# Performance work log

Hardware: AMD Instinct MI355X
Metric: run time of the kernel (lower is better)

## Reference

```python
import jax, jax.numpy as jnp
import numpy as np

N = 50000       # nodes
E = 800000      # edges (before self-loops)
F = 128         # input features
H = 4           # heads
C = 64          # hidden per head
NC = 40         # classes
NEG_SLOPE = 0.2  # PyG GATConv default leaky relu slope


def _glorot(key, shape):
    fan = sum(shape[-2:]) if len(shape) >= 2 else shape[-1] * 2
    return jax.random.normal(key, shape, jnp.float32) * jnp.sqrt(2.0 / fan)


def gat_conv(x, W, a_src, a_dst, bias, src, dst, concat):
    """PyG-style GATConv (eval mode, self-loops already in src/dst).
    x:[N,Fin] W:[Fin,H*C] a_src,a_dst:[H,C] bias:[H*C] or [C]."""
    n = x.shape[0]
    h_, c_ = a_src.shape
    h = (x @ W).reshape(n, h_, c_)                      # [N,H,C]
    al_s = jnp.einsum('nhc,hc->nh', h, a_src)           # [N,H]
    al_d = jnp.einsum('nhc,hc->nh', h, a_dst)
    logits = jax.nn.leaky_relu(al_s[src] + al_d[dst], NEG_SLOPE)  # [E,H]
    # segment softmax over incoming edges of each dst node
    mx = jax.ops.segment_max(logits, dst, num_segments=n)
    mx = jnp.where(jnp.isfinite(mx), mx, 0.0)
    ex = jnp.exp(logits - mx[dst])
    den = jax.ops.segment_sum(ex, dst, num_segments=n)
    alpha = ex / (den[dst] + 1e-16)                     # [E,H]
    msg = h[src] * alpha[:, :, None]                    # [E,H,C]
    out = jax.ops.segment_sum(msg, dst, num_segments=n) # [N,H,C]
    if concat:
        return out.reshape(n, h_ * c_) + bias
    return out.mean(axis=1) + bias


def setup_inputs() -> dict:
    key = jax.random.key(0)
    ks = jax.random.split(key, 16)
    x = jax.random.normal(ks[0], (N, F), jnp.float32)
    edge_index = jax.random.randint(ks[1], (2, E), 0, N, jnp.int64)
    HC = H * C
    return {
        'x': x, 'edge_index': edge_index,
        'W1': _glorot(ks[2], (F, HC)),   'a1_src': _glorot(ks[3], (H, C)),
        'a1_dst': _glorot(ks[4], (H, C)), 'b1': jnp.zeros((HC,), jnp.float32),
        'W2': _glorot(ks[5], (HC, HC)),  'a2_src': _glorot(ks[6], (H, C)),
        'a2_dst': _glorot(ks[7], (H, C)), 'b2': jnp.zeros((HC,), jnp.float32),
        'W3': _glorot(ks[8], (HC, H * NC)), 'a3_src': _glorot(ks[9], (H, NC)),
        'a3_dst': _glorot(ks[10], (H, NC)), 'b3': jnp.zeros((NC,), jnp.float32),
    }


def reference(x, edge_index, W1, a1_src, a1_dst, b1, W2, a2_src, a2_dst, b2,
              W3, a3_src, a3_dst, b3):
    n = x.shape[0]
    loop = jnp.arange(n, dtype=edge_index.dtype)
    src = jnp.concatenate([edge_index[0], loop])
    dst = jnp.concatenate([edge_index[1], loop])
    x1 = jax.nn.elu(gat_conv(x, W1, a1_src, a1_dst, b1, src, dst, True))
    x2 = jax.nn.elu(gat_conv(x1, W2, a2_src, a2_dst, b2, src, dst, True) + x1)
    out = gat_conv(x2, W3, a3_src, a3_dst, b3, src, dst, False)  # [N,NC]
    return out
```

## Files before the change

### kernel.cpp

```cpp
#include <hip/hip_runtime.h>
#include <hip/hip_bf16.h>
#include <hip/hip_fp16.h>
#include <math.h>

#define NEG_SLOPE 0.2f

typedef _Float16 half8 __attribute__((ext_vector_type(8)));
typedef _Float16 half4 __attribute__((ext_vector_type(4)));
typedef float f32x4 __attribute__((ext_vector_type(4)));

__global__ __launch_bounds__(256) void prep_kernel(
        const float* __restrict__ x, _Float16* __restrict__ xh, int n4,
        const float* __restrict__ W1, const float* __restrict__ W2,
        const float* __restrict__ W3,
        _Float16* __restrict__ b1h, _Float16* __restrict__ b1l,
        _Float16* __restrict__ b2h, _Float16* __restrict__ b2l,
        _Float16* __restrict__ b3h, _Float16* __restrict__ b3l,
        const int* __restrict__ ei, int E, int n, int* __restrict__ deg,
        int nbSplit, int nbWt) {
    int b = blockIdx.x;
    if (b < nbSplit) {
        int i = b * 256 + threadIdx.x;
        if (i >= n4) return;
        float4 v = ((const float4*)x)[i];
        half4 h;
        h.x = (_Float16)v.x; h.y = (_Float16)v.y;
        h.z = (_Float16)v.z; h.w = (_Float16)v.w;
        ((half4*)xh)[i] = h;
    } else if (b < nbSplit + nbWt) {
        int idx = (b - nbSplit) * 256 + threadIdx.x;
        const float* W; _Float16 *bh, *bl; int K, N, li;
        if (idx < 256 * 128) {
            W = W1; bh = b1h; bl = b1l; K = 128; N = 256; li = idx;
        } else if (idx < 256 * 128 + 256 * 256) {
            W = W2; bh = b2h; bl = b2l; K = 256; N = 256; li = idx - 256 * 128;
        } else if (idx < 256 * 128 + 2 * 256 * 256) {
            W = W3; bh = b3h; bl = b3l; K = 256; N = 160; li = idx - 256 * 128 - 256 * 256;
        } else return;
        int nn = li / K, k = li % K;
        float v = (nn < N) ? W[(size_t)k * N + nn] : 0.f;
        _Float16 h = (_Float16)v;
        bh[li] = h;
        bl[li] = (_Float16)(v - (float)h);
    } else {
        int e = (b - nbSplit - nbWt) * 256 + threadIdx.x;
        int tot = E + n;
        if (e >= tot) return;
        int d = (e < E) ? ei[E + e] : (e - E);
        atomicAdd(&deg[d], 1);
    }
}

__global__ __launch_bounds__(1024) void scan_block(const int* __restrict__ deg,
                                                   int* __restrict__ row_off,
                                                   int* __restrict__ bsums, int n) {
    __shared__ int tmp[1024];
    int t = threadIdx.x;
    int idx = blockIdx.x * 1024 + t;
    int v = (idx < n) ? deg[idx] : 0;
    tmp[t] = v;
    __syncthreads();
    #pragma unroll
    for (int off = 1; off < 1024; off <<= 1) {
        int x = (t >= off) ? tmp[t - off] : 0;
        __syncthreads();
        tmp[t] += x;
        __syncthreads();
    }
    if (idx < n) row_off[idx] = tmp[t] - v;
    if (t == 1023) bsums[blockIdx.x] = tmp[1023];
}

__global__ __launch_bounds__(64) void scan_sums(int* __restrict__ bsums, int nb,
                                                int* __restrict__ row_off, int n) {
    int lane = threadIdx.x;
    int carry = 0;
    for (int base = 0; base < nb; base += 64) {
        int i = base + lane;
        int o = (i < nb) ? bsums[i] : 0;
        int v = o;
        #pragma unroll
        for (int off = 1; off < 64; off <<= 1) {
            int x = __shfl_up(v, off, 64);
            if (lane >= off) v += x;
        }
        if (i < nb) bsums[i] = carry + v - o;
        int tot = __shfl(v, 63, 64);
        carry += tot;
    }
    if (lane == 0) row_off[n] = carry;
}

__global__ __launch_bounds__(1024) void scan_add(int* __restrict__ row_off,
                                                 const int* __restrict__ bsums,
                                                 int* __restrict__ cursor, int n) {
    int idx = blockIdx.x * 1024 + threadIdx.x;
    if (idx < n) {
        int v = row_off[idx] + bsums[blockIdx.x];
        row_off[idx] = v;
        cursor[idx] = v;
    }
}

__global__ void scatter_kernel(const int* __restrict__ ei, int E, int n,
                               int* __restrict__ cursor, int* __restrict__ csr_src) {
    int e = blockIdx.x * 256 + threadIdx.x;
    int tot = E + n;
    if (e >= tot) return;
    int s, d;
    if (e < E) { s = ei[e]; d = ei[E + e]; } else { s = d = e - E; }
    int pos = atomicAdd(&cursor[d], 1);
    csr_src[pos] = s;
}

template <int NK, bool FUSE>
__global__ __launch_bounds__(256) void gemm_mfma(const _Float16* __restrict__ A16,
                                                 const _Float16* __restrict__ Bthi,
                                                 const _Float16* __restrict__ Btlo,
                                                 _Float16* __restrict__ Ch,
                                                 const float* __restrict__ a_src,
                                                 const float* __restrict__ a_dst,
                                                 float* __restrict__ als,
                                                 float* __restrict__ ald,
                                                 int M, int N) {
    constexpr int K = NK * 32;
    __shared__ _Float16 Ah[2][64 * 32];
    int t = threadIdx.x;
    int wave = t >> 6, lane = t & 63;
    int row0 = blockIdx.x * 64;

    auto lds_off = [](int m, int g0) -> int {
        int P = m >> 1;
        int gp = ((m & 1) << 2) | g0;
        return P * 64 + ((gp ^ (P & 7)) << 3);
    };

    int r0 = t >> 2, g0 = t & 3;
    int off0 = lds_off(r0, g0);
    bool mok = (row0 + r0) < M;
    const _Float16* aph = A16 + (size_t)(row0 + r0) * K + g0 * 8;

    half8 svh;
    auto stage_load = [&](int k0) {
        svh = (half8)(_Float16)0.f;
        if (mok) svh = *(const half8*)(aph + k0);
    };
    auto stage_write = [&](int buf) {
        *(half8*)(&Ah[buf][off0]) = svh;
    };

    const _Float16* bhp[4];
    const _Float16* blp[4];
    #pragma unroll
    for (int nf = 0; nf < 4; nf++) {
        int n = wave * 64 + nf * 16 + (lane & 15);
        bhp[nf] = Bthi + (size_t)n * K + (lane >> 4) * 8;
        blp[nf] = Btlo + (size_t)n * K + (lane >> 4) * 8;
    }

    f32x4 acc[4][4];
    #pragma unroll
    for (int i = 0; i < 4; i++)
        #pragma unroll
        for (int j = 0; j < 4; j++)
            acc[i][j] = (f32x4)0.f;

    stage_load(0);
    stage_write(0);
    __syncthreads();

    #pragma unroll
    for (int kt = 0; kt < NK; kt++) {
        int cur = kt & 1;
        int k0 = kt * 32;
        half8 bh[4], bl[4];
        #pragma unroll
        for (int nf = 0; nf < 4; nf++) {
            bh[nf] = *(const half8*)(bhp[nf] + k0);
            bl[nf] = *(const half8*)(blp[nf] + k0);
        }
        if (kt + 1 < NK) stage_load((kt + 1) * 32);

        half8 ah[4];
        #pragma unroll
        for (int mf = 0; mf < 4; mf++) {
            int m = mf * 16 + (lane & 15);
            int off = lds_off(m, lane >> 4);
            ah[mf] = *(half8*)(&Ah[cur][off]);
        }
        #pragma unroll
        for (int mf = 0; mf < 4; mf++)
            #pragma unroll
            for (int nf = 0; nf < 4; nf++) {
                acc[mf][nf] = __builtin_amdgcn_mfma_f32_16x16x32_f16(
                    ah[mf], bh[nf], acc[mf][nf], 0, 0, 0);
                acc[mf][nf] = __builtin_amdgcn_mfma_f32_16x16x32_f16(
                    ah[mf], bl[nf], acc[mf][nf], 0, 0, 0);
            }
        if (kt + 1 < NK) {
            stage_write(cur ^ 1);
            __syncthreads();
        }
    }

    #pragma unroll
    for (int mf = 0; mf < 4; mf++)
        #pragma unroll
        for (int nf = 0; nf < 4; nf++) {
            int col = wave * 64 + nf * 16 + (lane & 15);
            if (col >= N) continue;
            #pragma unroll
            for (int q = 0; q < 4; q++) {
                int row = row0 + mf * 16 + (lane >> 4) * 4 + q;
                if (row < M)
                    Ch[(size_t)row * N + col] = (_Float16)acc[mf][nf][q];
            }
        }

    if (FUSE) {
        float asv[4], adv[4];
        #pragma unroll
        for (int nf = 0; nf < 4; nf++) {
            int cih = nf * 16 + (lane & 15);
            asv[nf] = a_src[wave * 64 + cih];
            adv[nf] = a_dst[wave * 64 + cih];
        }
        #pragma unroll
        for (int mf = 0; mf < 4; mf++)
            #pragma unroll
            for (int q = 0; q < 4; q++) {
                float ss = 0.f, sd = 0.f;
                #pragma unroll
                for (int nf = 0; nf < 4; nf++) {
                    float v = acc[mf][nf][q];
                    ss = fmaf(v, asv[nf], ss);
                    sd = fmaf(v, adv[nf], sd);
                }
                #pragma unroll
                for (int off = 8; off >= 1; off >>= 1) {
                    ss += __shfl_xor(ss, off, 64);
                    sd += __shfl_xor(sd, off, 64);
                }
                int row = row0 + mf * 16 + (lane >> 4) * 4 + q;
                if ((lane & 15) == 0 && row < M) {
                    als[row * 4 + wave] = ss;
                    ald[row * 4 + wave] = sd;
                }
            }
    }
}

template <int C>
__global__ __launch_bounds__(256) void coef_kernel(const _Float16* __restrict__ h,
                                                   const float* __restrict__ a_src,
                                                   const float* __restrict__ a_dst,
                                                   float* __restrict__ als,
                                                   float* __restrict__ ald, int n) {
    int wave = threadIdx.x >> 6;
    int lane = threadIdx.x & 63;
    int node = blockIdx.x * 4 + wave;
    if (node >= n) return;
    const _Float16* hr = h + (size_t)node * (4 * C);
    float ps[4], pd[4];
    #pragma unroll
    for (int hh = 0; hh < 4; hh++) {
        float hv = (lane < C) ? (float)hr[hh * C + lane] : 0.f;
        float as_ = (lane < C) ? a_src[hh * C + lane] : 0.f;
        float ad_ = (lane < C) ? a_dst[hh * C + lane] : 0.f;
        ps[hh] = hv * as_;
        pd[hh] = hv * ad_;
    }
    #pragma unroll
    for (int off = 32; off >= 1; off >>= 1) {
        #pragma unroll
        for (int hh = 0; hh < 4; hh++) {
            ps[hh] += __shfl_xor(ps[hh], off, 64);
            pd[hh] += __shfl_xor(pd[hh], off, 64);
        }
    }
    if (lane == 0) {
        #pragma unroll
        for (int hh = 0; hh < 4; hh++) {
            als[node * 4 + hh] = ps[hh];
            ald[node * 4 + hh] = pd[hh];
        }
    }
}

template <int C, int MODE>
__global__ __launch_bounds__(256) void agg_kernel(const __half* __restrict__ hhp,
                                                  const float* __restrict__ als,
                                                  const float* __restrict__ ald,
                                                  const int* __restrict__ row_off,
                                                  const int* __restrict__ csr_src,
                                                  const float* __restrict__ bias,
                                                  const _Float16* __restrict__ rh,
                                                  float* __restrict__ outf,
                                                  _Float16* __restrict__ oh, int n) {
    constexpr int HC = 4 * C;
    constexpr int LPN = HC / 8;
    constexpr int LPH = C / 8;
    const _Float16* hh = (const _Float16*)hhp;

    int t = threadIdx.x;
    int wave = t >> 6, lane = t & 63;
    int l = lane & 31;
    int node = (blockIdx.x * 4 + wave) * 2 + (lane >> 5);
    bool nact = node < n;
    bool lact = nact && (l < LPN);
    int g = (l < LPN) ? (l / LPH) : 0;

    int rs = 0, cnt = 0;
    if (lact) {
        rs = row_off[node];
        cnt = row_off[node + 1] - rs;
    }
    float aldg = lact ? ald[node * 4 + g] : 0.f;

    float acc[8] = {};
    float den = 0.f;

    if (cnt > 0) {
        int sA[8];
        float avA[8];
        #pragma unroll
        for (int q = 0; q < 8; q++) {
            int idx = q < cnt ? q : cnt - 1;
            sA[q] = csr_src[rs + idx];
        }
        #pragma unroll
        for (int q = 0; q < 8; q++) avA[q] = als[sA[q] * 4 + g];

        for (int base = 0; base < cnt; base += 8) {
            half8 hv[8];
            #pragma unroll
            for (int q = 0; q < 8; q++)
                hv[q] = *(const half8*)(hh + (size_t)sA[q] * HC + l * 8);

            int sB[8];
            float avB[8];
            if (base + 8 < cnt) {
                #pragma unroll
                for (int q = 0; q < 8; q++) {
                    int idx = base + 8 + q; if (idx >= cnt) idx = cnt - 1;
                    sB[q] = csr_src[rs + idx];
                }
                #pragma unroll
                for (int q = 0; q < 8; q++) avB[q] = als[sB[q] * 4 + g];
            }

            float ex[8];
            #pragma unroll
            for (int q = 0; q < 8; q++) {
                float lg = avA[q] + aldg;
                lg = (lg > 0.f) ? lg : NEG_SLOPE * lg;
                float e = __expf(lg);
                ex[q] = (base + q < cnt) ? e : 0.f;
                den += ex[q];
            }
            #pragma unroll
            for (int q = 0; q < 8; q++) {
                #pragma unroll
                for (int k = 0; k < 8; k++)
                    acc[k] = fmaf(ex[q], (float)hv[q][k], acc[k]);
            }
            #pragma unroll
            for (int q = 0; q < 8; q++) { sA[q] = sB[q]; avA[q] = avB[q]; }
        }
    }

    float inv = 1.f / (den + 1e-16f);
    float v[8];
    #pragma unroll
    for (int k = 0; k < 8; k++) v[k] = acc[k] * inv;

    if (MODE == 2) {
        float vs[8];
        #pragma unroll
        for (int k = 0; k < 8; k++) vs[k] = v[k];
        #pragma unroll
        for (int k2 = 1; k2 < 4; k2++) {
            #pragma unroll
            for (int k = 0; k < 8; k++)
                vs[k] += __shfl(v[k], lane + 5 * k2, 64);
        }
        if (nact && l < 5) {
            float b[8];
            *(float4*)&b[0] = *(const float4*)(bias + l * 8);
            *(float4*)&b[4] = *(const float4*)(bias + l * 8 + 4);
            float o[8];
            #pragma unroll
            for (int k = 0; k < 8; k++) o[k] = vs[k] * 0.25f + b[k];
            *(float4*)(outf + (size_t)node * C + l * 8)     = make_float4(o[0], o[1], o[2], o[3]);
            *(float4*)(outf + (size_t)node * C + l * 8 + 4) = make_float4(o[4], o[5], o[6], o[7]);
        }
    } else {
        if (lact) {
            float b[8];
            *(float4*)&b[0] = *(const float4*)(bias + l * 8);
            *(float4*)&b[4] = *(const float4*)(bias + l * 8 + 4);
            float o[8];
            #pragma unroll
            for (int k = 0; k < 8; k++) o[k] = v[k] + b[k];
            if (MODE == 1) {
                size_t ridx = (size_t)node * HC + l * 8;
                half8 r_h = *(const half8*)(rh + ridx);
                #pragma unroll
                for (int k = 0; k < 8; k++) o[k] += (float)r_h[k];
            }
            #pragma unroll
            for (int k = 0; k < 8; k++) o[k] = (o[k] > 0.f) ? o[k] : expm1f(o[k]);
            half8 hv8;
            #pragma unroll
            for (int k = 0; k < 8; k++) hv8[k] = (_Float16)o[k];
            *(half8*)(oh + (size_t)node * HC + l * 8) = hv8;
        }
    }
}

extern "C" void kernel_launch(void* const* d_in, const int* in_sizes, int n_in,
                              void* d_out, int out_size, void* d_ws, size_t ws_size,
                              hipStream_t stream) {
    const float* x   = (const float*)d_in[0];
    const int*   ei  = (const int*)d_in[1];
    const float* W1  = (const float*)d_in[2];
    const float* a1s = (const float*)d_in[3];
    const float* a1d = (const float*)d_in[4];
    const float* b1  = (const float*)d_in[5];
    const float* W2  = (const float*)d_in[6];
    const float* a2s = (const float*)d_in[7];
    const float* a2d = (const float*)d_in[8];
    const float* b2  = (const float*)d_in[9];
    const float* W3  = (const float*)d_in[10];
    const float* a3s = (const float*)d_in[11];
    const float* a3d = (const float*)d_in[12];
    const float* b3  = (const float*)d_in[13];
    float* out = (float*)d_out;

    int N = in_sizes[0] / 128;
    int E = in_sizes[1] / 2;

    char* ws = (char*)d_ws;
    size_t off = 0;
    auto alloc = [&](size_t bytes) -> void* {
        void* p = ws + off;
        off += (bytes + 255) & ~(size_t)255;
        return p;
    };
    _Float16* hhalf = (_Float16*)alloc((size_t)N * 256 * 2);
    _Float16* pA    = (_Float16*)alloc((size_t)N * 256 * 2);
    _Float16* pB    = (_Float16*)alloc((size_t)N * 256 * 2);
    float*    als   = (float*)alloc((size_t)N * 4 * 4);
    float*    ald   = (float*)alloc((size_t)N * 4 * 4);
    _Float16* bt1h  = (_Float16*)alloc(256 * 128 * 2);
    _Float16* bt1l  = (_Float16*)alloc(256 * 128 * 2);
    _Float16* bt2h  = (_Float16*)alloc(256 * 256 * 2);
    _Float16* bt2l  = (_Float16*)alloc(256 * 256 * 2);
    _Float16* bt3h  = (_Float16*)alloc(256 * 256 * 2);
    _Float16* bt3l  = (_Float16*)alloc(256 * 256 * 2);
    int* deg     = (int*)alloc((size_t)N * 4);
    int* row_off = (int*)alloc((size_t)(N + 1) * 4);
    int* cursor  = (int*)alloc((size_t)N * 4);
    int* csr     = (int*)alloc((size_t)(E + N) * 4);
    int* bsums   = (int*)alloc(1024 * 4);

    int tot = E + N;
    int nb = (N + 1023) / 1024;
    int n4 = N * 128 / 4;
    int nbSplit = (n4 + 255) / 256;
    int wtot = 256 * 128 + 2 * 256 * 256;
    int nbWt = (wtot + 255) / 256;
    int nbDeg = (tot + 255) / 256;

    hipMemsetAsync(deg, 0, (size_t)N * 4, stream);
    prep_kernel<<<nbSplit + nbWt + nbDeg, 256, 0, stream>>>(
        x, pA, n4, W1, W2, W3,
        bt1h, bt1l, bt2h, bt2l, bt3h, bt3l,
        ei, E, N, deg, nbSplit, nbWt);
    scan_block<<<nb, 1024, 0, stream>>>(deg, row_off, bsums, N);
    scan_sums<<<1, 64, 0, stream>>>(bsums, nb, row_off, N);
    scan_add<<<nb, 1024, 0, stream>>>(row_off, bsums, cursor, N);
    scatter_kernel<<<(tot + 255) / 256, 256, 0, stream>>>(ei, E, N, cursor, csr);

    int nodeBlocks4 = (N + 3) / 4;
    int pairs = (N + 1) / 2;
    int aggBlocks = (pairs + 3) / 4;
    dim3 blk(256);
    dim3 ggrid((N + 63) / 64);

    gemm_mfma<4, true><<<ggrid, blk, 0, stream>>>(pA, bt1h, bt1l, hhalf,
                                                  a1s, a1d, als, ald, N, 256);
    agg_kernel<64, 0><<<aggBlocks, blk, 0, stream>>>((const __half*)hhalf, als, ald,
        row_off, csr, b1, nullptr, nullptr, pB, N);

    gemm_mfma<8, true><<<ggrid, blk, 0, stream>>>(pB, bt2h, bt2l, hhalf,
                                                  a2s, a2d, als, ald, N, 256);
    agg_kernel<64, 1><<<aggBlocks, blk, 0, stream>>>((const __half*)hhalf, als, ald,
        row_off, csr, b2, pB, nullptr, pA, N);

    gemm_mfma<8, false><<<ggrid, blk, 0, stream>>>(pA, bt3h, bt3l, hhalf,
                                                   nullptr, nullptr, nullptr, nullptr, N, 160);
    coef_kernel<40><<<nodeBlocks4, blk, 0, stream>>>(hhalf, a3s, a3d, als, ald, N);
    agg_kernel<40, 2><<<aggBlocks, blk, 0, stream>>>((const __half*)hhalf, als, ald,
        row_off, csr, b3, nullptr, out, nullptr, N);
}
```

Before: 434.3 us.

## Stage GEMM A tiles via direct global-to-LDS loads and fold block-sum scan

```diff
diff --git a/kernel.cpp b/kernel.cpp
--- a/kernel.cpp
+++ b/kernel.cpp
@@ -71,32 +71,22 @@
     if (t == 1023) bsums[blockIdx.x] = tmp[1023];
 }
 
-__global__ __launch_bounds__(64) void scan_sums(int* __restrict__ bsums, int nb,
-                                                int* __restrict__ row_off, int n) {
-    int lane = threadIdx.x;
-    int carry = 0;
-    for (int base = 0; base < nb; base += 64) {
-        int i = base + lane;
-        int o = (i < nb) ? bsums[i] : 0;
-        int v = o;
-        #pragma unroll
-        for (int off = 1; off < 64; off <<= 1) {
-            int x = __shfl_up(v, off, 64);
-            if (lane >= off) v += x;
-        }
-        if (i < nb) bsums[i] = carry + v - o;
-        int tot = __shfl(v, 63, 64);
-        carry += tot;
-    }
-    if (lane == 0) row_off[n] = carry;
-}
-
 __global__ __launch_bounds__(1024) void scan_add(int* __restrict__ row_off,
                                                  const int* __restrict__ bsums,
-                                                 int* __restrict__ cursor, int n) {
-    int idx = blockIdx.x * 1024 + threadIdx.x;
+                                                 int* __restrict__ cursor,
+                                                 int n, int total) {
+    __shared__ int carry_s;
+    int b = blockIdx.x;
+    if (threadIdx.x == 0) {
+        int c = 0;
+        for (int i = 0; i < b; i++) c += bsums[i];
+        carry_s = c;
+        if (b == 0) row_off[n] = total;
+    }
+    __syncthreads();
+    int idx = b * 1024 + threadIdx.x;
     if (idx < n) {
-        int v = row_off[idx] + bsums[blockIdx.x];
+        int v = row_off[idx] + carry_s;
         row_off[idx] = v;
         cursor[idx] = v;
     }
@@ -124,7 +114,7 @@
                                                  float* __restrict__ ald,
                                                  int M, int N) {
     constexpr int K = NK * 32;
-    __shared__ _Float16 Ah[2][64 * 32];
+    __shared__ _Float16 Ah[2][2048];
     int t = threadIdx.x;
     int wave = t >> 6, lane = t & 63;
     int row0 = blockIdx.x * 64;
@@ -135,18 +125,19 @@
         return P * 64 + ((gp ^ (P & 7)) << 3);
     };
 
-    int r0 = t >> 2, g0 = t & 3;
-    int off0 = lds_off(r0, g0);
-    bool mok = (row0 + r0) < M;
-    const _Float16* aph = A16 + (size_t)(row0 + r0) * K + g0 * 8;
-
-    half8 svh;
-    auto stage_load = [&](int k0) {
-        svh = (half8)(_Float16)0.f;
-        if (mok) svh = *(const half8*)(aph + k0);
-    };
-    auto stage_write = [&](int buf) {
-        *(half8*)(&Ah[buf][off0]) = svh;
+    int Pw = t >> 3;
+    int gpw = (t & 7) ^ (Pw & 7);
+    int m_w = 2 * Pw + (gpw >> 2);
+    int g0w = gpw & 3;
+    int grow = row0 + m_w;
+    if (grow >= M) grow = M - 1;
+    const _Float16* srcp = A16 + (size_t)grow * K + g0w * 8;
+
+    auto stage = [&](int buf, int k0) {
+        __builtin_amdgcn_global_load_lds(
+            (const __attribute__((address_space(1))) void*)(srcp + k0),
+            (__attribute__((address_space(3))) void*)(&Ah[buf][(size_t)wave * 512]),
+            16, 0, 0);
     };
 
     const _Float16* bhp[4];
@@ -165,13 +156,14 @@
         for (int j = 0; j < 4; j++)
             acc[i][j] = (f32x4)0.f;
 
-    stage_load(0);
-    stage_write(0);
+    stage(0, 0);
     __syncthreads();
 
     #pragma unroll
     for (int kt = 0; kt < NK; kt++) {
         int cur = kt & 1;
+        if (kt + 1 < NK) stage(cur ^ 1, (kt + 1) * 32);
+
         int k0 = kt * 32;
         half8 bh[4], bl[4];
         #pragma unroll
@@ -179,8 +171,6 @@
             bh[nf] = *(const half8*)(bhp[nf] + k0);
             bl[nf] = *(const half8*)(blp[nf] + k0);
         }
-        if (kt + 1 < NK) stage_load((kt + 1) * 32);
-
         half8 ah[4];
         #pragma unroll
         for (int mf = 0; mf < 4; mf++) {
@@ -197,10 +187,7 @@
                 acc[mf][nf] = __builtin_amdgcn_mfma_f32_16x16x32_f16(
                     ah[mf], bl[nf], acc[mf][nf], 0, 0, 0);
             }
-        if (kt + 1 < NK) {
-            stage_write(cur ^ 1);
-            __syncthreads();
-        }
+        if (kt + 1 < NK) __syncthreads();
     }
 
     #pragma unroll
@@ -478,8 +465,7 @@
         bt1h, bt1l, bt2h, bt2l, bt3h, bt3l,
         ei, E, N, deg, nbSplit, nbWt);
     scan_block<<<nb, 1024, 0, stream>>>(deg, row_off, bsums, N);
-    scan_sums<<<1, 64, 0, stream>>>(bsums, nb, row_off, N);
-    scan_add<<<nb, 1024, 0, stream>>>(row_off, bsums, cursor, N);
+    scan_add<<<nb, 1024, 0, stream>>>(row_off, bsums, cursor, N, tot);
     scatter_kernel<<<(tot + 255) / 256, 256, 0, stream>>>(ei, E, N, cursor, csr);
 
     int nodeBlocks4 = (N + 3) / 4;
```

Measured after the change: 433.1 us. Within noise of the previous version (-0.3%).
